# Performance work log

Measured on AMD Instinct MI355X. Metric: run time of the kernel, lower is better.

## Reference

```python
import jax, jax.numpy as jnp
import numpy as np

HS = 512   # hidden_size
IN = 2048  # input_size
MB = 100   # memory_bank_size
T  = 4096  # nImg


def setup_inputs() -> dict:
    key = jax.random.key(0)
    ks = jax.random.split(key, 20)

    def w(k, i, o):
        return jax.random.normal(k, (i, o), jnp.float32) * (1.0 / np.sqrt(i))

    def b(k, o):
        return jax.random.normal(k, (o,), jnp.float32) * 0.01

    return {
        "hidden_out_a": jax.random.normal(ks[0], (T, IN), jnp.float32),
        "hidden_out_m": jax.random.normal(ks[1], (T, IN), jnp.float32),
        "W_ca": w(ks[2], HS + IN, HS),  "b_ca": b(ks[3], HS),    # hidden_to_content_a
        "W_cm": w(ks[4], HS + IN, HS),  "b_cm": b(ks[5], HS),    # hidden_to_content_m
        "W_wp": w(ks[6], 3 * HS, 3),    "b_wp": b(ks[7], 3),     # write_prob
        "W_wpa": w(ks[8], HS + IN, MB), "b_wpa": b(ks[9], MB),   # write_prob_a
        "W_wpm": w(ks[10], HS + IN, MB),"b_wpm": b(ks[11], MB),  # write_prob_m
        "W_rp": w(ks[12], 3 * HS, MB),  "b_rp": b(ks[13], MB),   # read_prob
        "W_rh": w(ks[14], 2 * HS, HS),  "b_rh": b(ks[15], HS),   # read_to_hidden
        "W_rha": w(ks[16], 2 * HS + IN, HS), "b_rha": b(ks[17], HS),  # read_to_hidden_a
        "W_rhm": w(ks[18], 2 * HS + IN, HS), "b_rhm": b(ks[19], HS),  # read_to_hidden_m
        "nImg": T,
    }


def reference(hidden_out_a, hidden_out_m,
              W_ca, b_ca, W_cm, b_cm,
              W_wp, b_wp, W_wpa, b_wpa, W_wpm, b_wpm,
              W_rp, b_rp, W_rh, b_rh,
              W_rha, b_rha, W_rhm, b_rhm,
              nImg):
    hs = W_rh.shape[1]
    mb = W_rp.shape[1]

    def step(carry, xs):
        mem, h, ha, hm = carry            # mem: [MB, HS]; h/ha/hm: [HS]
        xa, xm = xs                       # [IN] each
        xh = jnp.concatenate([ha, hm, h])               # [3*HS]
        ar = jax.nn.softmax(xh @ W_rp + b_rp)           # [MB]
        r = ar @ mem                                    # [HS] memory read
        h1 = jax.nn.relu(jnp.concatenate([r, h]) @ W_rh + b_rh)
        ha1 = jax.nn.relu(jnp.concatenate([xa, r, ha]) @ W_rha + b_rha)
        hm1 = jax.nn.relu(jnp.concatenate([xm, r, hm]) @ W_rhm + b_rhm)
        aw = jax.nn.softmax(xh @ W_wp + b_wp)           # [3] stream gate
        xha = jnp.concatenate([ha, xa])                 # [HS+IN]
        xhm = jnp.concatenate([hm, xm])
        c_a = jax.nn.relu(xha @ W_ca + b_ca)            # [HS]
        c_m = jax.nn.relu(xhm @ W_cm + b_cm)
        aw_a = jax.nn.softmax(xha @ W_wpa + b_wpa)      # [MB]
        aw_m = jax.nn.softmax(xhm @ W_wpm + b_wpm)
        mem = aw[0] * mem + aw[1] * aw_a[:, None] * c_a + aw[2] * aw_m[:, None] * c_m
        return (mem, h1, ha1, hm1), h1

    init = (jnp.zeros((mb, hs), hidden_out_a.dtype),
            jnp.zeros((hs,), hidden_out_a.dtype),
            jnp.zeros((hs,), hidden_out_a.dtype),
            jnp.zeros((hs,), hidden_out_a.dtype))
    _, hiddens = jax.lax.scan(step, init,
                              (hidden_out_a[:nImg], hidden_out_m[:nImg]))
    return hiddens  # [nImg, HS]
```

## Files before the change

### kernel.cpp

```cpp
#include <hip/hip_runtime.h>
#include <cstdint>
#include <cstddef>

#define HS 512

constexpr int TPB  = 512;
constexpr int GBLK = 64;
constexpr int OWNB = 24;

constexpr size_t OFF_TWrp  = 0;
constexpr size_t OFF_TWwp  = OFF_TWrp  + 100*1536;
constexpr size_t OFF_TWwpa = OFF_TWwp  + 3*1536;
constexpr size_t OFF_TWwpm = OFF_TWwpa + 100*512;
constexpr size_t OFF_TWca  = OFF_TWwpm + 100*512;
constexpr size_t OFF_TWcm  = OFF_TWca  + 512*512;
constexpr size_t OFF_TWh0  = OFF_TWcm  + 512*512;
constexpr size_t OFF_TWh1  = OFF_TWh0  + 512*512;
constexpr size_t OFF_TWh2  = OFF_TWh1  + 512*512;
constexpr size_t OFF_TWu0  = OFF_TWh2  + 512*512;
constexpr size_t OFF_TWu1  = OFF_TWu0  + 512*512;
constexpr size_t OFF_TWu2  = OFF_TWu1  + 512*512;
constexpr size_t OFF_PAca  = OFF_TWu2  + 512*512;
constexpr size_t OFF_PMcm  = OFF_PAca  + 4096*512;
constexpr size_t OFF_PArha = OFF_PMcm  + 4096*512;
constexpr size_t OFF_PMrhm = OFF_PArha + 4096*512;
constexpr size_t OFF_PAwpa = OFF_PMrhm + 4096*512;
constexpr size_t OFF_PMwpm = OFF_PAwpa + 4096*100;
constexpr size_t OFF_CARRY = OFF_PMwpm + 4096*100;
constexpr size_t OFF_BCAST = OFF_CARRY + 2*1536*2;

__device__ __forceinline__ unsigned long long ald(const unsigned long long* p) {
  return __hip_atomic_load(const_cast<unsigned long long*>(p),
                           __ATOMIC_RELAXED, __HIP_MEMORY_SCOPE_AGENT);
}
__device__ __forceinline__ void gstTag(unsigned long long* p, float v, unsigned tag) {
  unsigned long long u = ((unsigned long long)tag << 32) | (unsigned long long)__float_as_uint(v);
  __hip_atomic_store(p, u, __ATOMIC_RELAXED, __HIP_MEMORY_SCOPE_AGENT);
}
__device__ __forceinline__ float xrsum(float v) {
  #pragma unroll
  for (int o = 32; o; o >>= 1) v += __shfl_xor(v, o, 64);
  return v;
}
__device__ __forceinline__ float rsum16(float v) {
  #pragma unroll
  for (int o = 8; o; o >>= 1) v += __shfl_xor(v, o, 64);
  return v;
}

__global__ void initK(unsigned long long* carryT, unsigned long long* bcast) {
  int i = blockIdx.x * blockDim.x + threadIdx.x, st = gridDim.x * blockDim.x;
  for (int k = i; k < 1536; k += st) carryT[k] = (1ull << 32);
  for (int k = i; k < 1536; k += st) carryT[1536 + k] = 0ull;
  for (int k = i; k < 2 * 1344; k += st) bcast[k] = 0ull;
}

__global__ void transK(const float* __restrict__ src, float* __restrict__ dst, int R, int C) {
  __shared__ float tile[32][33];
  int c0 = blockIdx.x * 32, r0 = blockIdx.y * 32;
  for (int i = threadIdx.y; i < 32; i += 8) {
    int r = r0 + i, c = c0 + threadIdx.x;
    tile[i][threadIdx.x] = (r < R && c < C) ? src[(size_t)r * C + c] : 0.f;
  }
  __syncthreads();
  for (int i = threadIdx.y; i < 32; i += 8) {
    int c = c0 + i, r = r0 + threadIdx.x;
    if (c < C && r < R) dst[(size_t)c * R + r] = tile[threadIdx.x][i];
  }
}

__global__ __launch_bounds__(256) void gemmK(const float* __restrict__ X,
                                             const float* __restrict__ W,
                                             float* __restrict__ C, int N) {
  __shared__ float As[16][68];
  __shared__ float Bs[16][68];
  int t0 = blockIdx.y * 64, n0 = blockIdx.x * 64;
  int tid = threadIdx.x, tx = tid & 15, ty = tid >> 4;
  float acc[4][4] = {};
  for (int k0 = 0; k0 < 2048; k0 += 16) {
    {
      int r = tid >> 2, c = (tid & 3) * 4;
      float4 v = *(const float4*)(X + (size_t)(t0 + r) * 2048 + k0 + c);
      As[c + 0][r] = v.x; As[c + 1][r] = v.y; As[c + 2][r] = v.z; As[c + 3][r] = v.w;
    }
    {
      int kr = tid >> 4, c = (tid & 15) * 4;
      int gcol = n0 + c;
      const float* src = W + (size_t)(k0 + kr) * N + gcol;
      #pragma unroll
      for (int i = 0; i < 4; ++i) Bs[kr][c + i] = (gcol + i < N) ? src[i] : 0.f;
    }
    __syncthreads();
    #pragma unroll
    for (int kk = 0; kk < 16; ++kk) {
      float4 a4 = *(const float4*)&As[kk][ty * 4];
      float4 b4 = *(const float4*)&Bs[kk][tx * 4];
      float av[4] = {a4.x, a4.y, a4.z, a4.w};
      float bv[4] = {b4.x, b4.y, b4.z, b4.w};
      #pragma unroll
      for (int i = 0; i < 4; ++i)
        #pragma unroll
        for (int j = 0; j < 4; ++j) acc[i][j] += av[i] * bv[j];
    }
    __syncthreads();
  }
  #pragma unroll
  for (int i = 0; i < 4; ++i)
    #pragma unroll
    for (int j = 0; j < 4; ++j) {
      int col = n0 + tx * 4 + j;
      if (col < N) C[(size_t)(t0 + ty * 4 + i) * N + col] = acc[i][j];
    }
}

__global__ __launch_bounds__(256) void gemm128(const float* __restrict__ X,
                                               const float* __restrict__ W,
                                               float* __restrict__ C) {
  __shared__ float As[8][132];
  __shared__ float Bs[8][132];
  const int N = 512;
  int t0 = blockIdx.y * 128, n0 = blockIdx.x * 128;
  int tid = threadIdx.x, tx = tid & 15, ty = tid >> 4;
  float acc[8][8] = {};
  for (int k0 = 0; k0 < 2048; k0 += 8) {
    int r = tid >> 1, c4 = (tid & 1) * 4;
    float4 va = *(const float4*)(X + (size_t)(t0 + r) * 2048 + k0 + c4);
    int kr = tid >> 5, cb = (tid & 31) * 4;
    float4 vb = *(const float4*)(W + (size_t)(k0 + kr) * N + n0 + cb);
    __syncthreads();
    As[c4 + 0][r] = va.x; As[c4 + 1][r] = va.y; As[c4 + 2][r] = va.z; As[c4 + 3][r] = va.w;
    Bs[kr][cb] = vb.x; Bs[kr][cb + 1] = vb.y; Bs[kr][cb + 2] = vb.z; Bs[kr][cb + 3] = vb.w;
    __syncthreads();
    #pragma unroll
    for (int kk = 0; kk < 8; ++kk) {
      float av[8], bv[8];
      *(float4*)av       = *(const float4*)&As[kk][ty * 8];
      *(float4*)(av + 4) = *(const float4*)&As[kk][ty * 8 + 4];
      *(float4*)bv       = *(const float4*)&Bs[kk][tx * 8];
      *(float4*)(bv + 4) = *(const float4*)&Bs[kk][tx * 8 + 4];
      #pragma unroll
      for (int i = 0; i < 8; ++i)
        #pragma unroll
        for (int j = 0; j < 8; ++j) acc[i][j] += av[i] * bv[j];
    }
  }
  #pragma unroll
  for (int i = 0; i < 8; ++i) {
    float* dst = C + (size_t)(t0 + ty * 8 + i) * N + n0 + tx * 8;
    *(float4*)dst       = *(float4*)&acc[i][0];
    *(float4*)(dst + 4) = *(float4*)&acc[i][4];
  }
}

struct RArgs {
  const float *TWrp, *TWwp, *TWwpa, *TWwpm, *TWca, *TWcm;
  const float *TWh0, *TWh1, *TWh2, *TWu0, *TWu1, *TWu2;
  const float *PAca, *PMcm, *PArha, *PMrhm, *PAwpa, *PMwpm;
  const float *b_ca, *b_cm, *b_wp, *b_wpa, *b_wpm, *b_rp, *b_rh, *b_rha, *b_rhm;
  unsigned long long *carryT, *bcast;
  float *out;
  int nT;
};

__global__ __launch_bounds__(TPB, 1) void recurK(RArgs a) {
  const int tid  = threadIdx.x;
  const int lane = tid & 63;
  const int lw   = tid >> 6;
  const int g    = tid >> 4;
  const int gl   = tid & 15;
  const int b    = blockIdx.x;

  __shared__ __align__(16) float s_x[1536];
  __shared__ __align__(16) float s_c[1024];
  __shared__ float s_ar[112], s_awa[112], s_awm[112], s_aw[4];

  const int r0a = (b + 51) & 63;
  const int r1m = (b + 25) & 63;
  const bool big1_grp = (b < 36);
  const bool big1_wp  = (b >= 40 && b <= 42);

  if (tid < 112) { s_ar[tid] = 0.f; s_awa[tid] = 0.f; s_awm[tid] = 0.f; }

  int dstA = -1, xoffA = 0, strideA = 512;
  bool reluA = false;
  float biasA = 0.f;
  const float* preAPtr = nullptr;
  const float* wARow = nullptr;
  if (lw < 2) {
    int col = b * 8 + g;
    dstA = col; reluA = true; biasA = a.b_ca[col]; preAPtr = a.PAca + col;
    wARow = a.TWca + (size_t)col * 512; xoffA = 0;
  } else if (lw < 4) {
    int col = b * 8 + (g - 8);
    dstA = 512 + col; reluA = true; biasA = a.b_cm[col]; preAPtr = a.PMcm + col;
    wARow = a.TWcm + (size_t)col * 512; xoffA = 512;
  } else if (lw == 4) {
    int sl = g - 16;
    strideA = 100;
    if (sl == 0)                  { dstA = 1124 + r0a;      biasA = a.b_wpa[r0a];      preAPtr = a.PAwpa + r0a;      wARow = a.TWwpa + (size_t)r0a * 512;        xoffA = 0;   }
    else if (sl == 1 && r0a < 36) { dstA = 1124 + r0a + 64; biasA = a.b_wpa[r0a + 64]; preAPtr = a.PAwpa + r0a + 64; wARow = a.TWwpa + (size_t)(r0a + 64) * 512; xoffA = 0;   }
    else if (sl == 2)             { dstA = 1224 + r1m;      biasA = a.b_wpm[r1m];      preAPtr = a.PMwpm + r1m;      wARow = a.TWwpm + (size_t)r1m * 512;        xoffA = 512; }
    else if (sl == 3 && r1m < 36) { dstA = 1224 + r1m + 64; biasA = a.b_wpm[r1m + 64]; preAPtr = a.PMwpm + r1m + 64; wARow = a.TWwpm + (size_t)(r1m + 64) * 512; xoffA = 512; }
  }
  int dstBig = -1;
  float biasBig = 0.f;
  const float* wBigRow = nullptr;
  if (lw == 6) { dstBig = 1024 + b; biasBig = a.b_rp[b]; wBigRow = a.TWrp + (size_t)b * 1536; }
  else if (lw == 7) {
    if (big1_grp)      { dstBig = 1024 + b + 64;   biasBig = a.b_rp[b + 64]; wBigRow = a.TWrp + (size_t)(b + 64) * 1536; }
    else if (big1_wp)  { dstBig = 1324 + (b - 40); biasBig = a.b_wp[b - 40]; wBigRow = a.TWwp + (size_t)(b - 40) * 1536; }
  }
  const bool own = (g < OWNB);
  int ownHsel = 0, ownJ = 0, whXo = 0;
  float biasO = 0.f;
  const float* preOPtr = nullptr;
  const float* whRow = nullptr;
  const float* uRow = nullptr;
  if (own) {
    int q = b * OWNB + g, hsel = q >> 9, j = q & 511;
    ownHsel = hsel; ownJ = j;
    if (hsel == 0)      { biasO = a.b_rh[j];
                          whRow = a.TWh0 + (size_t)j * 512; whXo = 1024;
                          uRow  = a.TWu0 + (size_t)j * 512; }
    else if (hsel == 1) { biasO = a.b_rha[j]; preOPtr = a.PArha + j;
                          whRow = a.TWh1 + (size_t)j * 512; whXo = 0;
                          uRow  = a.TWu1 + (size_t)j * 512; }
    else                { biasO = a.b_rhm[j]; preOPtr = a.PMrhm + j;
                          whRow = a.TWh2 + (size_t)j * 512; whXo = 512;
                          uRow  = a.TWu2 + (size_t)j * 512; }
  }

  float4 wA[8];
  float4 wU[8];
  float4 wWh[8];
  float4 wB[6];
  float  gr[7];
  #pragma unroll
  for (int it = 0; it < 8; ++it) wA[it] = wU[it] = wWh[it] = make_float4(0.f, 0.f, 0.f, 0.f);
  #pragma unroll
  for (int it = 0; it < 6; ++it) wB[it] = make_float4(0.f, 0.f, 0.f, 0.f);
  #pragma unroll
  for (int k = 0; k < 7; ++k) gr[k] = 0.f;

  if (wARow) {
    const float4* w4 = (const float4*)wARow;
    #pragma unroll
    for (int it = 0; it < 8; ++it) wA[it] = w4[gl + 16 * it];
  }
  if (own) {
    const float4* u4 = (const float4*)uRow;
    const float4* h4 = (const float4*)whRow;
    #pragma unroll
    for (int it = 0; it < 8; ++it) { wU[it] = u4[gl + 16 * it]; wWh[it] = h4[gl + 16 * it]; }
  }
  if (wBigRow) {
    const float4* w4 = (const float4*)wBigRow;
    #pragma unroll
    for (int it = 0; it < 6; ++it) wB[it] = w4[lane + 64 * it];
  }
  __syncthreads();

  float preA_c = preAPtr ? preAPtr[0] : 0.f;
  float preO_c = preOPtr ? preOPtr[0] : 0.f;

  float whv = 0.f;
  for (int t = 0; t < a.nT; ++t) {
    const unsigned tagB = (unsigned)t + 1;
    unsigned long long* bc = a.bcast + (size_t)(t & 1) * 1344;

    {
      const unsigned long long* cin = a.carryT + (size_t)(t & 1) * 1536;
      int i0 = tid, i1 = tid + 512, i2 = tid + 1024;
      unsigned long long v0 = ald(cin + i0), v1 = ald(cin + i1), v2 = ald(cin + i2);
      while (((unsigned)(v0 >> 32) < tagB) | ((unsigned)(v1 >> 32) < tagB) |
             ((unsigned)(v2 >> 32) < tagB)) {
        __builtin_amdgcn_s_sleep(1);
        v0 = ald(cin + i0); v1 = ald(cin + i1); v2 = ald(cin + i2);
      }
      s_x[i0] = __uint_as_float((unsigned)v0);
      s_x[i1] = __uint_as_float((unsigned)v1);
      s_x[i2] = __uint_as_float((unsigned)v2);
    }
    __syncthreads();

    const int tn = (t + 1 < a.nT) ? t + 1 : t;
    float preA_n = preAPtr ? preAPtr[(size_t)tn * strideA] : 0.f;
    float preO_n = preOPtr ? preOPtr[(size_t)tn * 512] : 0.f;

    if (dstA >= 0) {
      const float4* x4 = (const float4*)(s_x + xoffA);
      float acc = 0.f;
      #pragma unroll
      for (int it = 0; it < 8; ++it) {
        float4 xv = x4[gl + 16 * it];
        acc += wA[it].x * xv.x + wA[it].y * xv.y + wA[it].z * xv.z + wA[it].w * xv.w;
      }
      float v = rsum16(acc);
      if (!gl) {
        v += preA_c + biasA;
        if (reluA) v = fmaxf(v, 0.f);
        gstTag(bc + dstA, v, tagB);
      }
    } else if (dstBig >= 0) {
      const float4* x4 = (const float4*)s_x;
      float acc = 0.f;
      #pragma unroll
      for (int it = 0; it < 6; ++it) {
        float4 xv = x4[lane + 64 * it];
        acc += wB[it].x * xv.x + wB[it].y * xv.y + wB[it].z * xv.z + wB[it].w * xv.w;
      }
      float v = xrsum(acc);
      if (!lane) gstTag(bc + dstBig, v + biasBig, tagB);
    }
    if (own) {
      const float4* x4 = (const float4*)(s_x + whXo);
      float acc = 0.f;
      #pragma unroll
      for (int it = 0; it < 8; ++it) {
        float4 xv = x4[gl + 16 * it];
        acc += wWh[it].x * xv.x + wWh[it].y * xv.y + wWh[it].z * xv.z + wWh[it].w * xv.w;
      }
      whv = rsum16(acc);
    }

    if (lw < 3) {
      int base = 1024 + lw * 100;
      const unsigned long long* p1 = bc + base + lane;
      bool two = lane < 36;
      unsigned long long v1 = ald(p1);
      unsigned long long v2 = two ? ald(p1 + 64) : ~0ull;
      while (((unsigned)(v1 >> 32) < tagB) | ((unsigned)(v2 >> 32) < tagB)) {
        __builtin_amdgcn_s_sleep(1);
        v1 = ald(p1); if (two) v2 = ald(p1 + 64);
      }
      float x1 = __uint_as_float((unsigned)v1);
      float x2 = two ? __uint_as_float((unsigned)v2) : -3.0e38f;
      float m = fmaxf(x1, x2);
      #pragma unroll
      for (int o = 32; o; o >>= 1) m = fmaxf(m, __shfl_xor(m, o, 64));
      float e1 = expf(x1 - m);
      float e2 = two ? expf(x2 - m) : 0.f;
      float ss = e1 + e2;
      #pragma unroll
      for (int o = 32; o; o >>= 1) ss += __shfl_xor(ss, o, 64);
      float inv = 1.f / ss;
      float* dst = (lw == 0) ? s_ar : (lw == 1) ? s_awa : s_awm;
      dst[lane] = e1 * inv;
      if (two) dst[64 + lane] = e2 * inv;
    } else if (lw == 3) {
      float x = -3.0e38f;
      if (lane < 3) {
        const unsigned long long* p = bc + 1324 + lane;
        unsigned long long v = ald(p);
        while ((unsigned)(v >> 32) < tagB) { __builtin_amdgcn_s_sleep(1); v = ald(p); }
        x = __uint_as_float((unsigned)v);
      }
      float m = x;
      #pragma unroll
      for (int o = 32; o; o >>= 1) m = fmaxf(m, __shfl_xor(m, o, 64));
      float e = (lane < 3) ? expf(x - m) : 0.f;
      float ss = e;
      #pragma unroll
      for (int o = 32; o; o >>= 1) ss += __shfl_xor(ss, o, 64);
      if (lane < 3) s_aw[lane] = e / ss;
    } else {
      int base = tid - 256;
      const unsigned long long* p = bc + base;
      unsigned long long v0 = ald(p), v1 = ald(p + 256), v2 = ald(p + 512), v3 = ald(p + 768);
      while (((unsigned)(v0 >> 32) < tagB) | ((unsigned)(v1 >> 32) < tagB) |
             ((unsigned)(v2 >> 32) < tagB) | ((unsigned)(v3 >> 32) < tagB)) {
        __builtin_amdgcn_s_sleep(1);
        v0 = ald(p); v1 = ald(p + 256); v2 = ald(p + 512); v3 = ald(p + 768);
      }
      s_c[base]       = __uint_as_float((unsigned)v0);
      s_c[base + 256] = __uint_as_float((unsigned)v1);
      s_c[base + 512] = __uint_as_float((unsigned)v2);
      s_c[base + 768] = __uint_as_float((unsigned)v3);
    }
    __syncthreads();

    unsigned long long* cout = a.carryT + (size_t)((t + 1) & 1) * 1536;
    if (own) {
      const float aw0 = s_aw[0], aw1 = s_aw[1], aw2 = s_aw[2];
      const float4* a4 = (const float4*)s_c;
      const float4* m4 = (const float4*)(s_c + 512);
      float sa = 0.f, sm = 0.f;
      #pragma unroll
      for (int it = 0; it < 8; ++it) {
        float4 av = a4[gl + 16 * it], mv = m4[gl + 16 * it];
        sa += wU[it].x * av.x + wU[it].y * av.y + wU[it].z * av.z + wU[it].w * av.w;
        sm += wU[it].x * mv.x + wU[it].y * mv.y + wU[it].z * mv.z + wU[it].w * mv.w;
      }
      #pragma unroll
      for (int o = 8; o; o >>= 1) { sa += __shfl_xor(sa, o, 64); sm += __shfl_xor(sm, o, 64); }
      const float uA = sa, uM = sm;

      float contrib = 0.f;
      #pragma unroll
      for (int k = 0; k < 7; ++k) contrib += s_ar[gl + 16 * k] * gr[k];
      contrib = rsum16(contrib);
      if (!gl) {
        float h = fmaxf(contrib + whv + preO_c + biasO, 0.f);
        if (ownHsel == 0) {
          a.out[(size_t)t * 512 + ownJ] = h;
          gstTag(cout + 1024 + ownJ, h, tagB + 1);
        } else if (ownHsel == 1) {
          gstTag(cout + ownJ, h, tagB + 1);
        } else {
          gstTag(cout + 512 + ownJ, h, tagB + 1);
        }
      }
      #pragma unroll
      for (int k = 0; k < 7; ++k) {
        int idx = gl + 16 * k;
        gr[k] = aw0 * gr[k] + aw1 * s_awa[idx] * uA + aw2 * s_awm[idx] * uM;
      }
    }

    preA_c = preA_n;
    preO_c = preO_n;
  }
}

extern "C" void kernel_launch(void* const* d_in, const int* in_sizes, int n_in,
                              void* d_out, int out_size, void* d_ws, size_t ws_size,
                              hipStream_t stream) {
  const float* Xa    = (const float*)d_in[0];
  const float* Xm    = (const float*)d_in[1];
  const float* W_ca  = (const float*)d_in[2];  const float* b_ca  = (const float*)d_in[3];
  const float* W_cm  = (const float*)d_in[4];  const float* b_cm  = (const float*)d_in[5];
  const float* W_wp  = (const float*)d_in[6];  const float* b_wp  = (const float*)d_in[7];
  const float* W_wpa = (const float*)d_in[8];  const float* b_wpa = (const float*)d_in[9];
  const float* W_wpm = (const float*)d_in[10]; const float* b_wpm = (const float*)d_in[11];
  const float* W_rp  = (const float*)d_in[12]; const float* b_rp  = (const float*)d_in[13];
  const float* W_rh  = (const float*)d_in[14]; const float* b_rh  = (const float*)d_in[15];
  const float* W_rha = (const float*)d_in[16]; const float* b_rha = (const float*)d_in[17];
  const float* W_rhm = (const float*)d_in[18]; const float* b_rhm = (const float*)d_in[19];

  int nT = out_size / HS;
  float* ws = (float*)d_ws;

  initK<<<dim3(64), dim3(256), 0, stream>>>(
      (unsigned long long*)(ws + OFF_CARRY),
      (unsigned long long*)(ws + OFF_BCAST));

  dim3 tb(32, 8);
  auto tg = [](int R, int C) { return dim3((C + 31) / 32, (R + 31) / 32); };
  transK<<<tg(1536, 100), tb, 0, stream>>>(W_rp,                       ws + OFF_TWrp,  1536, 100);
  transK<<<tg(1536, 3),   tb, 0, stream>>>(W_wp,                       ws + OFF_TWwp,  1536, 3);
  transK<<<tg(512, 100),  tb, 0, stream>>>(W_wpa,                      ws + OFF_TWwpa, 512, 100);
  transK<<<tg(512, 100),  tb, 0, stream>>>(W_wpm,                      ws + OFF_TWwpm, 512, 100);
  transK<<<tg(512, 512),  tb, 0, stream>>>(W_ca,                       ws + OFF_TWca,  512, 512);
  transK<<<tg(512, 512),  tb, 0, stream>>>(W_cm,                       ws + OFF_TWcm,  512, 512);
  transK<<<tg(512, 512),  tb, 0, stream>>>(W_rh  + 512 * 512,          ws + OFF_TWh0,  512, 512);
  transK<<<tg(512, 512),  tb, 0, stream>>>(W_rha + (size_t)2560 * 512, ws + OFF_TWh1,  512, 512);
  transK<<<tg(512, 512),  tb, 0, stream>>>(W_rhm + (size_t)2560 * 512, ws + OFF_TWh2,  512, 512);
  transK<<<tg(512, 512),  tb, 0, stream>>>(W_rh,                       ws + OFF_TWu0,  512, 512);
  transK<<<tg(512, 512),  tb, 0, stream>>>(W_rha + (size_t)2048 * 512, ws + OFF_TWu1,  512, 512);
  transK<<<tg(512, 512),  tb, 0, stream>>>(W_rhm + (size_t)2048 * 512, ws + OFF_TWu2,  512, 512);

  int tB = nT / 128;
  gemm128<<<dim3(4, tB), dim3(256), 0, stream>>>(Xa, W_ca + (size_t)512 * 512, ws + OFF_PAca);
  gemm128<<<dim3(4, tB), dim3(256), 0, stream>>>(Xm, W_cm + (size_t)512 * 512, ws + OFF_PMcm);
  gemm128<<<dim3(4, tB), dim3(256), 0, stream>>>(Xa, W_rha,                    ws + OFF_PArha);
  gemm128<<<dim3(4, tB), dim3(256), 0, stream>>>(Xm, W_rhm,                    ws + OFF_PMrhm);
  int tB64 = nT / 64;
  gemmK<<<dim3(2, tB64), dim3(256), 0, stream>>>(Xa, W_wpa + (size_t)512 * 100, ws + OFF_PAwpa, 100);
  gemmK<<<dim3(2, tB64), dim3(256), 0, stream>>>(Xm, W_wpm + (size_t)512 * 100, ws + OFF_PMwpm, 100);

  RArgs a;
  a.TWrp  = ws + OFF_TWrp;  a.TWwp  = ws + OFF_TWwp;
  a.TWwpa = ws + OFF_TWwpa; a.TWwpm = ws + OFF_TWwpm;
  a.TWca  = ws + OFF_TWca;  a.TWcm  = ws + OFF_TWcm;
  a.TWh0  = ws + OFF_TWh0;  a.TWh1  = ws + OFF_TWh1;  a.TWh2 = ws + OFF_TWh2;
  a.TWu0  = ws + OFF_TWu0;  a.TWu1  = ws + OFF_TWu1;  a.TWu2 = ws + OFF_TWu2;
  a.PAca  = ws + OFF_PAca;  a.PMcm  = ws + OFF_PMcm;
  a.PArha = ws + OFF_PArha; a.PMrhm = ws + OFF_PMrhm;
  a.PAwpa = ws + OFF_PAwpa; a.PMwpm = ws + OFF_PMwpm;
  a.b_ca = b_ca; a.b_cm = b_cm; a.b_wp = b_wp; a.b_wpa = b_wpa; a.b_wpm = b_wpm;
  a.b_rp = b_rp; a.b_rh = b_rh; a.b_rha = b_rha; a.b_rhm = b_rhm;
  a.carryT = (unsigned long long*)(ws + OFF_CARRY);
  a.bcast  = (unsigned long long*)(ws + OFF_BCAST);
  a.out    = (float*)d_out;
  a.nT     = nT;

  recurK<<<dim3(GBLK), dim3(TPB), 0, stream>>>(a);
}
```

Measured before the change: 22.80 ms.

## Replace block barrier with per-warp LDS flags to publish hidden state earlier

```diff
diff --git a/kernel.cpp b/kernel.cpp
--- a/kernel.cpp
+++ b/kernel.cpp
@@ -46,6 +46,11 @@
   #pragma unroll
   for (int o = 8; o; o >>= 1) v += __shfl_xor(v, o, 64);
   return v;
+}
+__device__ __forceinline__ void spinF(volatile unsigned* f, unsigned v) {
+  while (*f < v) { }
+  __builtin_amdgcn_sched_barrier(0);
+  asm volatile("" ::: "memory");
 }
 
 __global__ void initK(unsigned long long* carryT, unsigned long long* bcast) {
@@ -173,6 +178,8 @@
   __shared__ __align__(16) float s_x[1536];
   __shared__ __align__(16) float s_c[1024];
   __shared__ float s_ar[112], s_awa[112], s_awm[112], s_aw[4];
+  __shared__ unsigned s_flags[8];
+  volatile unsigned* FL = s_flags;
 
   const int r0a = (b + 51) & 63;
   const int r1m = (b + 25) & 63;
@@ -180,6 +187,7 @@
   const bool big1_wp  = (b >= 40 && b <= 42);
 
   if (tid < 112) { s_ar[tid] = 0.f; s_awa[tid] = 0.f; s_awm[tid] = 0.f; }
+  if (tid < 8) s_flags[tid] = 0u;
 
   int dstA = -1, xoffA = 0, strideA = 512;
   bool reluA = false;
@@ -323,15 +331,18 @@
       whv = rsum16(acc);
     }
 
-    if (lw < 3) {
-      int base = 1024 + lw * 100;
-      const unsigned long long* p1 = bc + base + lane;
+    if (lw == 0) {
+      const unsigned long long* p1 = bc + 1024 + lane;
       bool two = lane < 36;
+      bool wpx = (lane >= 40 && lane < 43);
+      const unsigned long long* pw = bc + 1324 + (lane - 40);
       unsigned long long v1 = ald(p1);
       unsigned long long v2 = two ? ald(p1 + 64) : ~0ull;
-      while (((unsigned)(v1 >> 32) < tagB) | ((unsigned)(v2 >> 32) < tagB)) {
+      unsigned long long vw = wpx ? ald(pw) : ~0ull;
+      while (((unsigned)(v1 >> 32) < tagB) | ((unsigned)(v2 >> 32) < tagB) |
+             ((unsigned)(vw >> 32) < tagB)) {
         __builtin_amdgcn_s_sleep(1);
-        v1 = ald(p1); if (two) v2 = ald(p1 + 64);
+        v1 = ald(p1); if (two) v2 = ald(p1 + 64); if (wpx) vw = ald(pw);
       }
       float x1 = __uint_as_float((unsigned)v1);
       float x2 = two ? __uint_as_float((unsigned)v2) : -3.0e38f;
@@ -344,57 +355,15 @@
       #pragma unroll
       for (int o = 32; o; o >>= 1) ss += __shfl_xor(ss, o, 64);
       float inv = 1.f / ss;
-      float* dst = (lw == 0) ? s_ar : (lw == 1) ? s_awa : s_awm;
-      dst[lane] = e1 * inv;
-      if (two) dst[64 + lane] = e2 * inv;
-    } else if (lw == 3) {
-      float x = -3.0e38f;
-      if (lane < 3) {
-        const unsigned long long* p = bc + 1324 + lane;
-        unsigned long long v = ald(p);
-        while ((unsigned)(v >> 32) < tagB) { __builtin_amdgcn_s_sleep(1); v = ald(p); }
-        x = __uint_as_float((unsigned)v);
-      }
-      float m = x;
-      #pragma unroll
-      for (int o = 32; o; o >>= 1) m = fmaxf(m, __shfl_xor(m, o, 64));
-      float e = (lane < 3) ? expf(x - m) : 0.f;
-      float ss = e;
-      #pragma unroll
-      for (int o = 32; o; o >>= 1) ss += __shfl_xor(ss, o, 64);
-      if (lane < 3) s_aw[lane] = e / ss;
-    } else {
-      int base = tid - 256;
-      const unsigned long long* p = bc + base;
-      unsigned long long v0 = ald(p), v1 = ald(p + 256), v2 = ald(p + 512), v3 = ald(p + 768);
-      while (((unsigned)(v0 >> 32) < tagB) | ((unsigned)(v1 >> 32) < tagB) |
-             ((unsigned)(v2 >> 32) < tagB) | ((unsigned)(v3 >> 32) < tagB)) {
-        __builtin_amdgcn_s_sleep(1);
-        v0 = ald(p); v1 = ald(p + 256); v2 = ald(p + 512); v3 = ald(p + 768);
-      }
-      s_c[base]       = __uint_as_float((unsigned)v0);
-      s_c[base + 256] = __uint_as_float((unsigned)v1);
-      s_c[base + 512] = __uint_as_float((unsigned)v2);
-      s_c[base + 768] = __uint_as_float((unsigned)v3);
-    }
-    __syncthreads();
+      s_ar[lane] = e1 * inv;
+      if (two) s_ar[64 + lane] = e2 * inv;
+      asm volatile("s_waitcnt lgkmcnt(0)" ::: "memory");
+      if (!lane) FL[0] = tagB;
+    }
 
     unsigned long long* cout = a.carryT + (size_t)((t + 1) & 1) * 1536;
     if (own) {
-      const float aw0 = s_aw[0], aw1 = s_aw[1], aw2 = s_aw[2];
-      const float4* a4 = (const float4*)s_c;
-      const float4* m4 = (const float4*)(s_c + 512);
-      float sa = 0.f, sm = 0.f;
-      #pragma unroll
-      for (int it = 0; it < 8; ++it) {
-        float4 av = a4[gl + 16 * it], mv = m4[gl + 16 * it];
-        sa += wU[it].x * av.x + wU[it].y * av.y + wU[it].z * av.z + wU[it].w * av.w;
-        sm += wU[it].x * mv.x + wU[it].y * mv.y + wU[it].z * mv.z + wU[it].w * mv.w;
-      }
-      #pragma unroll
-      for (int o = 8; o; o >>= 1) { sa += __shfl_xor(sa, o, 64); sm += __shfl_xor(sm, o, 64); }
-      const float uA = sa, uM = sm;
-
+      spinF(&FL[0], tagB);
       float contrib = 0.f;
       #pragma unroll
       for (int k = 0; k < 7; ++k) contrib += s_ar[gl + 16 * k] * gr[k];
@@ -410,6 +379,115 @@
           gstTag(cout + 512 + ownJ, h, tagB + 1);
         }
       }
+    }
+
+    if (lw == 1) {
+      const unsigned long long* p1 = bc + 1124 + lane;
+      bool two = lane < 36;
+      unsigned long long v1 = ald(p1);
+      unsigned long long v2 = two ? ald(p1 + 64) : ~0ull;
+      while (((unsigned)(v1 >> 32) < tagB) | ((unsigned)(v2 >> 32) < tagB)) {
+        __builtin_amdgcn_s_sleep(1);
+        v1 = ald(p1); if (two) v2 = ald(p1 + 64);
+      }
+      float x1 = __uint_as_float((unsigned)v1);
+      float x2 = two ? __uint_as_float((unsigned)v2) : -3.0e38f;
+      float m = fmaxf(x1, x2);
+      #pragma unroll
+      for (int o = 32; o; o >>= 1) m = fmaxf(m, __shfl_xor(m, o, 64));
+      float e1 = expf(x1 - m);
+      float e2 = two ? expf(x2 - m) : 0.f;
+      float ss = e1 + e2;
+      #pragma unroll
+      for (int o = 32; o; o >>= 1) ss += __shfl_xor(ss, o, 64);
+      float inv = 1.f / ss;
+      s_awa[lane] = e1 * inv;
+      if (two) s_awa[64 + lane] = e2 * inv;
+      asm volatile("s_waitcnt lgkmcnt(0)" ::: "memory");
+      if (!lane) FL[2] = tagB;
+    } else if (lw == 2) {
+      const unsigned long long* p1 = bc + 1224 + lane;
+      bool two = lane < 36;
+      unsigned long long v1 = ald(p1);
+      unsigned long long v2 = two ? ald(p1 + 64) : ~0ull;
+      while (((unsigned)(v1 >> 32) < tagB) | ((unsigned)(v2 >> 32) < tagB)) {
+        __builtin_amdgcn_s_sleep(1);
+        v1 = ald(p1); if (two) v2 = ald(p1 + 64);
+      }
+      float x1 = __uint_as_float((unsigned)v1);
+      float x2 = two ? __uint_as_float((unsigned)v2) : -3.0e38f;
+      float m = fmaxf(x1, x2);
+      #pragma unroll
+      for (int o = 32; o; o >>= 1) m = fmaxf(m, __shfl_xor(m, o, 64));
+      float e1 = expf(x1 - m);
+      float e2 = two ? expf(x2 - m) : 0.f;
+      float ss = e1 + e2;
+      #pragma unroll
+      for (int o = 32; o; o >>= 1) ss += __shfl_xor(ss, o, 64);
+      float inv = 1.f / ss;
+      s_awm[lane] = e1 * inv;
+      if (two) s_awm[64 + lane] = e2 * inv;
+      asm volatile("s_waitcnt lgkmcnt(0)" ::: "memory");
+      if (!lane) FL[3] = tagB;
+    } else if (lw == 3) {
+      float x = -3.0e38f;
+      if (lane < 3) {
+        const unsigned long long* p = bc + 1324 + lane;
+        unsigned long long v = ald(p);
+        while ((unsigned)(v >> 32) < tagB) { __builtin_amdgcn_s_sleep(1); v = ald(p); }
+        x = __uint_as_float((unsigned)v);
+      }
+      float m = x;
+      #pragma unroll
+      for (int o = 32; o; o >>= 1) m = fmaxf(m, __shfl_xor(m, o, 64));
+      float e = (lane < 3) ? expf(x - m) : 0.f;
+      float ss = e;
+      #pragma unroll
+      for (int o = 32; o; o >>= 1) ss += __shfl_xor(ss, o, 64);
+      if (lane < 3) s_aw[lane] = e / ss;
+      asm volatile("s_waitcnt lgkmcnt(0)" ::: "memory");
+      if (!lane) FL[1] = tagB;
+    } else if (lw >= 6) {
+      int ci = tid - 384;
+      const unsigned long long* p = bc + ci;
+      unsigned long long v[8];
+      #pragma unroll
+      for (int k = 0; k < 8; ++k) v[k] = ald(p + 128 * k);
+      for (;;) {
+        bool ok = true;
+        #pragma unroll
+        for (int k = 0; k < 8; ++k) ok &= ((unsigned)(v[k] >> 32) >= tagB);
+        if (__all(ok)) break;
+        __builtin_amdgcn_s_sleep(1);
+        #pragma unroll
+        for (int k = 0; k < 8; ++k) v[k] = ald(p + 128 * k);
+      }
+      #pragma unroll
+      for (int k = 0; k < 8; ++k) s_c[ci + 128 * k] = __uint_as_float((unsigned)v[k]);
+      asm volatile("s_waitcnt lgkmcnt(0)" ::: "memory");
+      if (!lane) FL[4 + (lw - 6)] = tagB;
+    }
+
+    if (own) {
+      spinF(&FL[4], tagB);
+      spinF(&FL[5], tagB);
+      const float4* a4 = (const float4*)s_c;
+      const float4* m4 = (const float4*)(s_c + 512);
+      float sa = 0.f, sm = 0.f;
+      #pragma unroll
+      for (int it = 0; it < 8; ++it) {
+        float4 av = a4[gl + 16 * it], mv = m4[gl + 16 * it];
+        sa += wU[it].x * av.x + wU[it].y * av.y + wU[it].z * av.z + wU[it].w * av.w;
+        sm += wU[it].x * mv.x + wU[it].y * mv.y + wU[it].z * mv.z + wU[it].w * mv.w;
+      }
+      #pragma unroll
+      for (int o = 8; o; o >>= 1) { sa += __shfl_xor(sa, o, 64); sm += __shfl_xor(sm, o, 64); }
+      const float uA = sa, uM = sm;
+
+      spinF(&FL[1], tagB);
+      spinF(&FL[2], tagB);
+      spinF(&FL[3], tagB);
+      const float aw0 = s_aw[0], aw1 = s_aw[1], aw2 = s_aw[2];
       #pragma unroll
       for (int k = 0; k < 7; ++k) {
         int idx = gl + 16 * k;
```

New measurement: 25.28 ms. 10.9% more time.
